# Performance work log

Hardware: AMD Instinct MI355X
Metric: run time of the kernel (lower is better)

Reference implementation:

```python
import jax, jax.numpy as jnp
import numpy as np

B, H, S, C, D = 8, 32, 64, 4096, 128


def setup_inputs() -> dict:
    key = jax.random.key(0)
    k1, k2, k3, k4 = jax.random.split(key, 4)
    history = jax.random.randint(k1, (B, H, S), 0, C)
    current_trajectory = jax.random.randint(k2, (B, S), 0, C)
    E = jax.random.normal(k3, (B, C, D), dtype=jnp.float32)
    W_gcn = jax.random.normal(k4, (D, D), dtype=jnp.float32) * 0.05
    b_gcn = jnp.zeros((D,), dtype=jnp.float32)
    return {"candidate_size": C, "history": history,
            "current_trajectory": current_trajectory, "E": E,
            "W_gcn": W_gcn, "b_gcn": b_gcn}


def _temporal_embeddings(seq_len, embed_dim, dtype):
    # sinusoidal: e_t[2k] = sin(t / 10000^(2k/embed_dim)), e_t[2k+1] = cos(...)
    d = embed_dim // 2
    t = jnp.arange(seq_len, dtype=dtype)[:, None]            # [S,1]
    k = jnp.arange(d, dtype=dtype)[None, :]                  # [1,d]
    ang = t / (10000.0 ** (2.0 * k / embed_dim))             # [S,d]
    return jnp.stack([jnp.sin(ang), jnp.cos(ang)], axis=-1).reshape(seq_len, embed_dim)


def reference(candidate_size, history, current_trajectory, E, W_gcn, b_gcn):
    Bs, Hs, Ss = history.shape
    Cc = candidate_size
    dt = E.dtype
    # ---- get_graph: binary transition adjacency (torch advanced-index += is non-accumulating) ----
    h1 = history[:, :, :-1]
    h2 = history[:, :, 1:]
    m = (h1 != h2).astype(dt)                                # [B,H,S-1]
    b_idx = jnp.arange(Bs)[:, None, None]
    A = jnp.zeros((Bs, Cc, Cc), dtype=dt).at[b_idx, h1, h2].add(m)
    A = jnp.minimum(A, 1.0)
    # ---- Mytransform: A+I, then D @ A @ D with D = diag(sqrt(sum over dim=1)) ----
    A = A + jnp.eye(Cc, dtype=dt)
    s = jnp.sqrt(A.sum(axis=1))                              # [B,C]
    A = s[:, :, None] * A * s[:, None, :]
    # ---- GCN aggregate + relu(Linear) ----
    Eg = jax.nn.relu(jnp.einsum('bij,bjd->bid', A, E) @ W_gcn.T + b_gcn)
    pos = jnp.concatenate([Eg, E], axis=-1)                  # [B,C,2D]
    # ---- temporal embeddings + gather/add fusion ----
    te = _temporal_embeddings(Ss, pos.shape[-1], dt)         # [S,2D]
    fused_hist = pos[b_idx, history] + te[None, None, :, :]  # [B,H,S,2D]
    fused_cur = pos[jnp.arange(Bs)[:, None], current_trajectory] + te[None]  # [B,S,2D]
    fused_hist = fused_hist.reshape(Bs * Hs, Ss, -1)
    return fused_hist, fused_cur
```

## Files before the change

### kernel.cpp

```cpp
#include <hip/hip_runtime.h>

#define BB 8
#define HH 32
#define SS 64
#define CC 4096
#define DD 128
#define MAXU 2176

typedef __attribute__((ext_vector_type(8))) short bf16x8;
typedef __attribute__((ext_vector_type(4))) float f32x4;

__device__ inline unsigned short f32_to_bf16_rtn(float f) {
    unsigned u = __float_as_uint(f);
    u += 0x7FFFu + ((u >> 16) & 1u);
    return (unsigned short)(u >> 16);
}
__device__ inline float bf16lo(unsigned u) { return __uint_as_float(u << 16); }
__device__ inline float bf16hi(unsigned u) { return __uint_as_float(u & 0xFFFF0000u); }


__global__ __launch_bounds__(1024) void mega(const int* __restrict__ hist,
                                             const int* __restrict__ cur,
                                             const float* __restrict__ E,
                                             const float* __restrict__ W,
                                             unsigned* __restrict__ rowptr,
                                             unsigned* __restrict__ adj,
                                             float* __restrict__ s,
                                             unsigned* __restrict__ inv,
                                             unsigned* __restrict__ nused,
                                             unsigned* __restrict__ occp,
                                             unsigned* __restrict__ occ_list,
                                             float* __restrict__ te,
                                             unsigned short* __restrict__ EWb) {
    extern __shared__ unsigned smem_u[];
    const int tid = threadIdx.x;

    if (blockIdx.x >= BB + 16) {
        unsigned short* Abf = (unsigned short*)smem_u;
        unsigned short* Wb  = Abf + 64 * 136;
        const int r0 = (blockIdx.x - BB - 16) * 64;
        for (int idx = tid; idx < 2048; idx += 1024) {
            int row = idx >> 5, c4 = idx & 31;
            float4 v = ((const float4*)E)[(size_t)(r0 + row) * 32 + c4];
            ushort4 o;
            o.x = f32_to_bf16_rtn(v.x); o.y = f32_to_bf16_rtn(v.y);
            o.z = f32_to_bf16_rtn(v.z); o.w = f32_to_bf16_rtn(v.w);
            *(ushort4*)&Abf[row * 136 + c4 * 4] = o;
        }
        for (int idx = tid; idx < 4096; idx += 1024) {
            int n = idx >> 5, c4 = idx & 31;
            float4 v = ((const float4*)W)[idx];
            ushort4 o;
            o.x = f32_to_bf16_rtn(v.x); o.y = f32_to_bf16_rtn(v.y);
            o.z = f32_to_bf16_rtn(v.z); o.w = f32_to_bf16_rtn(v.w);
            *(ushort4*)&Wb[n * 136 + c4 * 4] = o;
        }
        __syncthreads();
        const int lane = tid & 63, wv = tid >> 6;
        const int l15 = lane & 15, l4 = lane >> 4;
        const int rb = (wv >> 2) * 16;
        const int cb = (wv & 3) * 32;
        f32x4 acc[2] = {{0.f, 0.f, 0.f, 0.f}, {0.f, 0.f, 0.f, 0.f}};
#pragma unroll
        for (int kt = 0; kt < 4; ++kt) {
            bf16x8 a = *(const bf16x8*)&Abf[(rb + l15) * 136 + kt * 32 + l4 * 8];
#pragma unroll
            for (int nt = 0; nt < 2; ++nt) {
                bf16x8 bb = *(const bf16x8*)&Wb[(cb + nt * 16 + l15) * 136 + kt * 32 + l4 * 8];
                acc[nt] = __builtin_amdgcn_mfma_f32_16x16x32_bf16(a, bb, acc[nt], 0, 0, 0);
            }
        }
#pragma unroll
        for (int nt = 0; nt < 2; ++nt) {
            int col = cb + nt * 16 + l15;
#pragma unroll
            for (int i = 0; i < 4; ++i) {
                int row = r0 + rb + l4 * 4 + i;
                EWb[(size_t)row * 128 + col] = f32_to_bf16_rtn(acc[nt][i]);
            }
        }
        return;
    }
    if (blockIdx.x >= BB) {
        int g = (blockIdx.x - BB) * 1024 + tid;
        int t = g >> 8, c = g & 255, k = c >> 1;
        float ang = (float)t * powf(10000.0f, -(float)k / 128.0f);
        te[g] = (c & 1) ? cosf(ang) : sinf(ang);
        return;
    }

    unsigned* table  = smem_u;
    unsigned* cntAB  = table + 4096;
    unsigned* cntOcc = cntAB + 4096;
    unsigned* pref   = cntOcc + 4096;
    unsigned* lkeys  = pref + 4096;
    unsigned* wbase  = lkeys + 2048;
    unsigned* totalp = wbase + 17;
    const int b = blockIdx.x;
    const int lane = tid & 63, wv = tid >> 6;

#pragma unroll
    for (int r = 0; r < 4; ++r) {
        int g = tid + r * 1024;
        table[g] = 0xFFFFFFFFu;
        cntAB[g] = 0u;
        cntOcc[g] = 0u;
    }
    if (tid == 0) *totalp = 0u;
    __syncthreads();

    for (int t = tid; t < HH * SS; t += 1024) atomicAdd(&cntOcc[hist[b * HH * SS + t]], 1u);
    if (tid < SS) atomicAdd(&cntOcc[cur[b * SS + tid]], 1u);

    for (int t = tid; t < HH * (SS - 1); t += 1024) {
        int h = t / 63, ss = t - h * 63;
        int base = (b * HH + h) * SS + ss;
        int i = hist[base], j = hist[base + 1];
        if (i != j) {
            unsigned key = ((unsigned)i << 12) | (unsigned)j;
            unsigned hh = (key * 2654435761u) >> 20;
            for (;;) {
                hh &= 4095u;
                unsigned old = atomicCAS(&table[hh], 0xFFFFFFFFu, key);
                if (old == 0xFFFFFFFFu) {
                    unsigned slot = atomicAdd(totalp, 1u);
                    lkeys[slot] = key;
                    atomicAdd(&cntAB[key & 4095u], 1u);
                    atomicAdd(&cntAB[key >> 12], 1u << 16);
                    break;
                }
                if (old == key) break;
                ++hh;
            }
        }
    }
    __syncthreads();

#pragma unroll
    for (int r = 0; r < 4; ++r) {
        int g = tid + r * 1024;
        s[b * CC + g] = sqrtf(1.0f + (float)(cntAB[g] & 0xFFFFu));
    }

    {
        unsigned v0 = ((cntAB[tid * 4]     >> 16) << 13) | (cntOcc[tid * 4]     ? 1u : 0u);
        unsigned v1 = ((cntAB[tid * 4 + 1] >> 16) << 13) | (cntOcc[tid * 4 + 1] ? 1u : 0u);
        unsigned v2 = ((cntAB[tid * 4 + 2] >> 16) << 13) | (cntOcc[tid * 4 + 2] ? 1u : 0u);
        unsigned v3 = ((cntAB[tid * 4 + 3] >> 16) << 13) | (cntOcc[tid * 4 + 3] ? 1u : 0u);
        unsigned tsum = v0 + v1 + v2 + v3;
        unsigned x = tsum;
#pragma unroll
        for (int off = 1; off < 64; off <<= 1) {
            unsigned y = __shfl_up(x, off);
            if (lane >= off) x += y;
        }
        if (lane == 63) wbase[wv + 1] = x;
        __syncthreads();
        if (tid == 0) {
            wbase[0] = 0u;
            for (int w = 1; w <= 16; ++w) wbase[w] += wbase[w - 1];
        }
        __syncthreads();
        unsigned texcl = wbase[wv] + x - tsum;
        pref[tid * 4]     = texcl;
        pref[tid * 4 + 1] = texcl + v0;
        pref[tid * 4 + 2] = texcl + v0 + v1;
        pref[tid * 4 + 3] = texcl + v0 + v1 + v2;
        __syncthreads();
#pragma unroll
        for (int r = 0; r < 4; ++r) {
            int g = tid + r * 1024;
            unsigned p = pref[g];
            rowptr[b * 4104 + g] = p >> 13;
            if (cntOcc[g]) inv[b * MAXU + (p & 8191u)] = (unsigned)g;
        }
        if (tid == 0) {
            rowptr[b * 4104 + 4096] = wbase[16] >> 13;
            nused[b] = wbase[16] & 8191u;
        }
    }
    __syncthreads();
#pragma unroll
    for (int r = 0; r < 4; ++r) cntAB[tid + r * 1024] = 0u;
    __syncthreads();

    {
        unsigned total = *totalp;
        for (int e = tid; e < (int)total; e += 1024) {
            unsigned key = lkeys[e];
            unsigned i = key >> 12, j = key & 4095u;
            unsigned pos = (pref[i] >> 13) + atomicAdd(&cntAB[i], 1u);
            adj[b * 2048 + pos] = j;
        }
    }
    __syncthreads();

    {
        unsigned v0 = cntOcc[tid * 4], v1 = cntOcc[tid * 4 + 1];
        unsigned v2 = cntOcc[tid * 4 + 2], v3 = cntOcc[tid * 4 + 3];
        unsigned tsum = v0 + v1 + v2 + v3;
        unsigned x = tsum;
#pragma unroll
        for (int off = 1; off < 64; off <<= 1) {
            unsigned y = __shfl_up(x, off);
            if (lane >= off) x += y;
        }
        if (lane == 63) wbase[wv + 1] = x;
        __syncthreads();
        if (tid == 0) {
            wbase[0] = 0u;
            for (int w = 1; w <= 16; ++w) wbase[w] += wbase[w - 1];
        }
        __syncthreads();
        unsigned texcl = wbase[wv] + x - tsum;
        pref[tid * 4]     = texcl;
        pref[tid * 4 + 1] = texcl + v0;
        pref[tid * 4 + 2] = texcl + v0 + v1;
        pref[tid * 4 + 3] = texcl + v0 + v1 + v2;
        __syncthreads();
#pragma unroll
        for (int r = 0; r < 4; ++r) {
            int g = tid + r * 1024;
            occp[b * 4104 + g] = pref[g];
        }
        if (tid == 0) occp[b * 4104 + 4096] = wbase[16];
    }
    __syncthreads();
#pragma unroll
    for (int r = 0; r < 4; ++r) cntAB[tid + r * 1024] = 0u;
    __syncthreads();

    for (int t = tid; t < HH * SS; t += 1024) {
        int cand = hist[b * HH * SS + t];
        unsigned pos = pref[cand] + atomicAdd(&cntAB[cand], 1u);
        occ_list[b * MAXU + pos] = ((unsigned)(b * 2048 + t) << 6) | (unsigned)(t & 63);
    }
    if (tid < SS) {
        int cand = cur[b * SS + tid];
        unsigned pos = pref[cand] + atomicAdd(&cntAB[cand], 1u);
        occ_list[b * MAXU + pos] =
            ((unsigned)(BB * HH * SS + b * SS + tid) << 6) | (unsigned)tid;
    }
}

__global__ __launch_bounds__(256) void apply_scatter(const float* __restrict__ E,
                                                     const float* __restrict__ s,
                                                     const unsigned* __restrict__ rowptr,
                                                     const unsigned* __restrict__ adj,
                                                     const unsigned* __restrict__ inv,
                                                     const unsigned* __restrict__ nused,
                                                     const unsigned short* __restrict__ EWb,
                                                     const float* __restrict__ bg,
                                                     const unsigned* __restrict__ occp,
                                                     const unsigned* __restrict__ occ_list,
                                                     const float* __restrict__ te,
                                                     float* __restrict__ out) {
    const int b = blockIdx.x / (MAXU / 4);
    const int slot = (blockIdx.x % (MAXU / 4)) * 4 + (threadIdx.x >> 6);
    const int lane = threadIdx.x & 63;
    if ((unsigned)slot >= nused[b]) return;
    const unsigned c = inv[b * MAXU + slot];
    const float si = s[b * CC + c];
    const unsigned* ew = (const unsigned*)EWb;

    unsigned u = ew[(size_t)(b * CC + c) * 64 + lane];
    float ax = si * bf16lo(u), ay = si * bf16hi(u);
    unsigned p0 = rowptr[b * 4104 + c], p1 = rowptr[b * 4104 + c + 1];
    for (unsigned p = p0; p < p1; ++p) {
        unsigned j = adj[b * 2048 + p];
        float sj = s[b * CC + j];
        unsigned uj = ew[(size_t)(b * CC + j) * 64 + lane];
        ax += sj * bf16lo(uj);
        ay += sj * bf16hi(uj);
    }
    float2 bgv = ((const float2*)bg)[lane];
    ax = fmaxf(si * ax + bgv.x, 0.f);
    ay = fmaxf(si * ay + bgv.y, 0.f);
    float2 e = ((const float2*)E)[(size_t)(b * CC + c) * 64 + lane];

    const float2* te2 = (const float2*)te;
    float2* out2 = (float2*)out;
    unsigned o0 = occp[b * 4104 + c], o1 = occp[b * 4104 + c + 1];
    for (unsigned o = o0; o < o1; ++o) {
        unsigned ent = occ_list[b * MAXU + o];
        unsigned outrow = ent >> 6, spos = ent & 63u;
        float2 t0 = te2[spos * 128 + lane];
        float2 t1 = te2[spos * 128 + 64 + lane];
        out2[(size_t)outrow * 128 + lane]      = make_float2(ax + t0.x, ay + t0.y);
        out2[(size_t)outrow * 128 + 64 + lane] = make_float2(e.x + t1.x, e.y + t1.y);
    }
}

extern "C" void kernel_launch(void* const* d_in, const int* in_sizes, int n_in,
                              void* d_out, int out_size, void* d_ws, size_t ws_size,
                              hipStream_t stream) {
    const int*   hist = (const int*)d_in[1];
    const int*   cur  = (const int*)d_in[2];
    const float* E    = (const float*)d_in[3];
    const float* W    = (const float*)d_in[4];
    const float* bg   = (const float*)d_in[5];
    float* out = (float*)d_out;

    unsigned* ws_u     = (unsigned*)d_ws;
    unsigned* rowptr   = ws_u;
    unsigned* adj      = rowptr + 32832;
    float*    sarr     = (float*)(adj + 16384);
    float*    te       = sarr + 32768;
    unsigned* inv      = (unsigned*)(te + 16384);
    unsigned* nused    = inv + 17408;
    unsigned* occp     = nused + 64;
    unsigned* occ_list = occp + 32832;
    unsigned short* EWb = (unsigned short*)(occ_list + 17408);

    mega<<<BB + 16 + 512, 1024, 73856, stream>>>(hist, cur, E, W, rowptr, adj,
                                                 sarr, inv, nused, occp,
                                                 occ_list, te, EWb);
    apply_scatter<<<BB * (MAXU / 4), 256, 0, stream>>>(E, sarr, rowptr, adj, inv,
                                                       nused, EWb, bg, occp,
                                                       occ_list, te, out);
}
```

Measured before the change: 30.49 us.

## Replace per-candidate scatter with direct per-output-row gather in apply kernel

Drops the occupancy counting, second prefix scan and occurrence-list build from the per-batch graph block. The apply kernel now launches one wavefront per output row, reads the candidate id straight from history/current, and recomputes that candidate's sparse aggregation rather than computing it once per unique candidate and scattering. This shortens the serial per-batch block and shrinks its LDS use, but repeats the adjacency aggregation for candidates that appear more than once.

New measurement: 25.60 us. -16.0%, faster.

```diff
diff --git a/kernel.cpp b/kernel.cpp
--- a/kernel.cpp
+++ b/kernel.cpp
@@ -5,7 +5,6 @@
 #define SS 64
 #define CC 4096
 #define DD 128
-#define MAXU 2176
 
 typedef __attribute__((ext_vector_type(8))) short bf16x8;
 typedef __attribute__((ext_vector_type(4))) float f32x4;
@@ -26,10 +25,6 @@
                                              unsigned* __restrict__ rowptr,
                                              unsigned* __restrict__ adj,
                                              float* __restrict__ s,
-                                             unsigned* __restrict__ inv,
-                                             unsigned* __restrict__ nused,
-                                             unsigned* __restrict__ occp,
-                                             unsigned* __restrict__ occ_list,
                                              float* __restrict__ te,
                                              unsigned short* __restrict__ EWb) {
     extern __shared__ unsigned smem_u[];
@@ -89,12 +84,10 @@
         return;
     }
 
-    unsigned* table  = smem_u;
-    unsigned* cntAB  = table + 4096;
-    unsigned* cntOcc = cntAB + 4096;
-    unsigned* pref   = cntOcc + 4096;
-    unsigned* lkeys  = pref + 4096;
-    unsigned* wbase  = lkeys + 2048;
+    unsigned* table = smem_u;
+    unsigned* cnt   = table + 4096;
+    unsigned* lkeys = cnt + 4096;
+    unsigned* wbase = lkeys + 2048;
     unsigned* totalp = wbase + 17;
     const int b = blockIdx.x;
     const int lane = tid & 63, wv = tid >> 6;
@@ -103,14 +96,10 @@
     for (int r = 0; r < 4; ++r) {
         int g = tid + r * 1024;
         table[g] = 0xFFFFFFFFu;
-        cntAB[g] = 0u;
-        cntOcc[g] = 0u;
+        cnt[g] = 0u;
     }
     if (tid == 0) *totalp = 0u;
     __syncthreads();
-
-    for (int t = tid; t < HH * SS; t += 1024) atomicAdd(&cntOcc[hist[b * HH * SS + t]], 1u);
-    if (tid < SS) atomicAdd(&cntOcc[cur[b * SS + tid]], 1u);
 
     for (int t = tid; t < HH * (SS - 1); t += 1024) {
         int h = t / 63, ss = t - h * 63;
@@ -125,8 +114,8 @@
                 if (old == 0xFFFFFFFFu) {
                     unsigned slot = atomicAdd(totalp, 1u);
                     lkeys[slot] = key;
-                    atomicAdd(&cntAB[key & 4095u], 1u);
-                    atomicAdd(&cntAB[key >> 12], 1u << 16);
+                    atomicAdd(&cnt[key & 4095u], 1u);
+                    atomicAdd(&cnt[key >> 12], 1u << 16);
                     break;
                 }
                 if (old == key) break;
@@ -139,14 +128,15 @@
 #pragma unroll
     for (int r = 0; r < 4; ++r) {
         int g = tid + r * 1024;
-        s[b * CC + g] = sqrtf(1.0f + (float)(cntAB[g] & 0xFFFFu));
-    }
-
+        s[b * CC + g] = sqrtf(1.0f + (float)(cnt[g] & 0xFFFFu));
+    }
+
+    unsigned* pref = table;
     {
-        unsigned v0 = ((cntAB[tid * 4]     >> 16) << 13) | (cntOcc[tid * 4]     ? 1u : 0u);
-        unsigned v1 = ((cntAB[tid * 4 + 1] >> 16) << 13) | (cntOcc[tid * 4 + 1] ? 1u : 0u);
-        unsigned v2 = ((cntAB[tid * 4 + 2] >> 16) << 13) | (cntOcc[tid * 4 + 2] ? 1u : 0u);
-        unsigned v3 = ((cntAB[tid * 4 + 3] >> 16) << 13) | (cntOcc[tid * 4 + 3] ? 1u : 0u);
+        unsigned v0 = cnt[tid * 4]     >> 16;
+        unsigned v1 = cnt[tid * 4 + 1] >> 16;
+        unsigned v2 = cnt[tid * 4 + 2] >> 16;
+        unsigned v3 = cnt[tid * 4 + 3] >> 16;
         unsigned tsum = v0 + v1 + v2 + v3;
         unsigned x = tsum;
 #pragma unroll
@@ -170,18 +160,13 @@
 #pragma unroll
         for (int r = 0; r < 4; ++r) {
             int g = tid + r * 1024;
-            unsigned p = pref[g];
-            rowptr[b * 4104 + g] = p >> 13;
-            if (cntOcc[g]) inv[b * MAXU + (p & 8191u)] = (unsigned)g;
-        }
-        if (tid == 0) {
-            rowptr[b * 4104 + 4096] = wbase[16] >> 13;
-            nused[b] = wbase[16] & 8191u;
-        }
-    }
-    __syncthreads();
-#pragma unroll
-    for (int r = 0; r < 4; ++r) cntAB[tid + r * 1024] = 0u;
+            rowptr[b * 4104 + g] = pref[g];
+        }
+        if (tid == 0) rowptr[b * 4104 + 4096] = wbase[16];
+    }
+    __syncthreads();
+#pragma unroll
+    for (int r = 0; r < 4; ++r) cnt[tid + r * 1024] = 0u;
     __syncthreads();
 
     {
@@ -189,83 +174,40 @@
         for (int e = tid; e < (int)total; e += 1024) {
             unsigned key = lkeys[e];
             unsigned i = key >> 12, j = key & 4095u;
-            unsigned pos = (pref[i] >> 13) + atomicAdd(&cntAB[i], 1u);
+            unsigned pos = pref[i] + atomicAdd(&cnt[i], 1u);
             adj[b * 2048 + pos] = j;
         }
     }
-    __syncthreads();
-
-    {
-        unsigned v0 = cntOcc[tid * 4], v1 = cntOcc[tid * 4 + 1];
-        unsigned v2 = cntOcc[tid * 4 + 2], v3 = cntOcc[tid * 4 + 3];
-        unsigned tsum = v0 + v1 + v2 + v3;
-        unsigned x = tsum;
-#pragma unroll
-        for (int off = 1; off < 64; off <<= 1) {
-            unsigned y = __shfl_up(x, off);
-            if (lane >= off) x += y;
-        }
-        if (lane == 63) wbase[wv + 1] = x;
-        __syncthreads();
-        if (tid == 0) {
-            wbase[0] = 0u;
-            for (int w = 1; w <= 16; ++w) wbase[w] += wbase[w - 1];
-        }
-        __syncthreads();
-        unsigned texcl = wbase[wv] + x - tsum;
-        pref[tid * 4]     = texcl;
-        pref[tid * 4 + 1] = texcl + v0;
-        pref[tid * 4 + 2] = texcl + v0 + v1;
-        pref[tid * 4 + 3] = texcl + v0 + v1 + v2;
-        __syncthreads();
-#pragma unroll
-        for (int r = 0; r < 4; ++r) {
-            int g = tid + r * 1024;
-            occp[b * 4104 + g] = pref[g];
-        }
-        if (tid == 0) occp[b * 4104 + 4096] = wbase[16];
-    }
-    __syncthreads();
-#pragma unroll
-    for (int r = 0; r < 4; ++r) cntAB[tid + r * 1024] = 0u;
-    __syncthreads();
-
-    for (int t = tid; t < HH * SS; t += 1024) {
-        int cand = hist[b * HH * SS + t];
-        unsigned pos = pref[cand] + atomicAdd(&cntAB[cand], 1u);
-        occ_list[b * MAXU + pos] = ((unsigned)(b * 2048 + t) << 6) | (unsigned)(t & 63);
-    }
-    if (tid < SS) {
-        int cand = cur[b * SS + tid];
-        unsigned pos = pref[cand] + atomicAdd(&cntAB[cand], 1u);
-        occ_list[b * MAXU + pos] =
-            ((unsigned)(BB * HH * SS + b * SS + tid) << 6) | (unsigned)tid;
-    }
-}
-
-__global__ __launch_bounds__(256) void apply_scatter(const float* __restrict__ E,
-                                                     const float* __restrict__ s,
-                                                     const unsigned* __restrict__ rowptr,
-                                                     const unsigned* __restrict__ adj,
-                                                     const unsigned* __restrict__ inv,
-                                                     const unsigned* __restrict__ nused,
-                                                     const unsigned short* __restrict__ EWb,
-                                                     const float* __restrict__ bg,
-                                                     const unsigned* __restrict__ occp,
-                                                     const unsigned* __restrict__ occ_list,
-                                                     const float* __restrict__ te,
-                                                     float* __restrict__ out) {
-    const int b = blockIdx.x / (MAXU / 4);
-    const int slot = (blockIdx.x % (MAXU / 4)) * 4 + (threadIdx.x >> 6);
-    const int lane = threadIdx.x & 63;
-    if ((unsigned)slot >= nused[b]) return;
-    const unsigned c = inv[b * MAXU + slot];
-    const float si = s[b * CC + c];
+}
+
+__global__ __launch_bounds__(256) void apply_out(const int* __restrict__ hist,
+                                                 const int* __restrict__ cur,
+                                                 const float* __restrict__ E,
+                                                 const float* __restrict__ s,
+                                                 const unsigned* __restrict__ rowptr,
+                                                 const unsigned* __restrict__ adj,
+                                                 const unsigned short* __restrict__ EWb,
+                                                 const float* __restrict__ bg,
+                                                 const float* __restrict__ te,
+                                                 float* __restrict__ out) {
+    const int g = blockIdx.x * 256 + threadIdx.x;
+    const int row = g >> 6, lane = g & 63;
+    int b, spos, cand;
+    if (row < BB * HH * SS) {
+        spos = row & 63;
+        b = row >> 11;
+        cand = hist[row];
+    } else {
+        int rc = row - BB * HH * SS;
+        spos = rc & 63;
+        b = rc >> 6;
+        cand = cur[rc];
+    }
     const unsigned* ew = (const unsigned*)EWb;
-
-    unsigned u = ew[(size_t)(b * CC + c) * 64 + lane];
+    const float si = s[b * CC + cand];
+    unsigned u = ew[(size_t)(b * CC + cand) * 64 + lane];
     float ax = si * bf16lo(u), ay = si * bf16hi(u);
-    unsigned p0 = rowptr[b * 4104 + c], p1 = rowptr[b * 4104 + c + 1];
+    unsigned p0 = rowptr[b * 4104 + cand], p1 = rowptr[b * 4104 + cand + 1];
     for (unsigned p = p0; p < p1; ++p) {
         unsigned j = adj[b * 2048 + p];
         float sj = s[b * CC + j];
@@ -276,19 +218,14 @@
     float2 bgv = ((const float2*)bg)[lane];
     ax = fmaxf(si * ax + bgv.x, 0.f);
     ay = fmaxf(si * ay + bgv.y, 0.f);
-    float2 e = ((const float2*)E)[(size_t)(b * CC + c) * 64 + lane];
+    float2 e = ((const float2*)E)[(size_t)(b * CC + cand) * 64 + lane];
 
     const float2* te2 = (const float2*)te;
+    float2 t0 = te2[spos * 128 + lane];
+    float2 t1 = te2[spos * 128 + 64 + lane];
     float2* out2 = (float2*)out;
-    unsigned o0 = occp[b * 4104 + c], o1 = occp[b * 4104 + c + 1];
-    for (unsigned o = o0; o < o1; ++o) {
-        unsigned ent = occ_list[b * MAXU + o];
-        unsigned outrow = ent >> 6, spos = ent & 63u;
-        float2 t0 = te2[spos * 128 + lane];
-        float2 t1 = te2[spos * 128 + 64 + lane];
-        out2[(size_t)outrow * 128 + lane]      = make_float2(ax + t0.x, ay + t0.y);
-        out2[(size_t)outrow * 128 + 64 + lane] = make_float2(e.x + t1.x, e.y + t1.y);
-    }
+    out2[(size_t)row * 128 + lane]      = make_float2(ax + t0.x, ay + t0.y);
+    out2[(size_t)row * 128 + 64 + lane] = make_float2(e.x + t1.x, e.y + t1.y);
 }
 
 extern "C" void kernel_launch(void* const* d_in, const int* in_sizes, int n_in,
@@ -301,21 +238,15 @@
     const float* bg   = (const float*)d_in[5];
     float* out = (float*)d_out;
 
-    unsigned* ws_u     = (unsigned*)d_ws;
-    unsigned* rowptr   = ws_u;
-    unsigned* adj      = rowptr + 32832;
-    float*    sarr     = (float*)(adj + 16384);
-    float*    te       = sarr + 32768;
-    unsigned* inv      = (unsigned*)(te + 16384);
-    unsigned* nused    = inv + 17408;
-    unsigned* occp     = nused + 64;
-    unsigned* occ_list = occp + 32832;
-    unsigned short* EWb = (unsigned short*)(occ_list + 17408);
-
-    mega<<<BB + 16 + 512, 1024, 73856, stream>>>(hist, cur, E, W, rowptr, adj,
-                                                 sarr, inv, nused, occp,
-                                                 occ_list, te, EWb);
-    apply_scatter<<<BB * (MAXU / 4), 256, 0, stream>>>(E, sarr, rowptr, adj, inv,
-                                                       nused, EWb, bg, occp,
-                                                       occ_list, te, out);
-}
+    unsigned* ws_u   = (unsigned*)d_ws;
+    unsigned* rowptr = ws_u;
+    unsigned* adj    = rowptr + 32832;
+    float*    sarr   = (float*)(adj + 16384);
+    float*    te     = sarr + 32768;
+    unsigned short* EWb = (unsigned short*)(te + 16384);
+
+    mega<<<BB + 16 + 512, 1024, 52224, stream>>>(hist, cur, E, W, rowptr, adj,
+                                                 sarr, te, EWb);
+    apply_out<<<(BB * HH * SS + BB * SS) / 4, 256, 0, stream>>>(
+        hist, cur, E, sarr, rowptr, adj, EWb, bg, te, out);
+}
```
